# Optimization experiments

Measured on AMD Instinct MI355X. Metric: run time of the kernel, lower is better.

Reference implementation:

```python
import jax, jax.numpy as jnp
import numpy as np

B, L, D = 32, 512, 384
T_MAX = 4096
PAD_VALUE = 0.0
EXPAND_SCALE = 1.0


def setup_inputs() -> dict:
    key = jax.random.key(0)
    k1, k2, k3 = jax.random.split(key, 3)
    sequence = jax.random.normal(k1, (B, L, D), dtype=jnp.float32)
    duration = jax.random.randint(k2, (B, L), 0, 8, dtype=jnp.int64)
    padding_mask = jax.random.randint(k3, (B, L), 0, 2) == 1
    return {"sequence": sequence, "duration": duration,
            "padding_mask": padding_mask, "max_length": T_MAX}


def reference(sequence, duration, padding_mask, max_length):
    # expanded_duration = round(expand_scale * duration)
    exp_dur = jnp.round(EXPAND_SCALE * duration.astype(jnp.float32)).astype(jnp.int32)
    # mask padded tokens in the input sequence with pad_value
    seq = jnp.where(padding_mask[..., None], PAD_VALUE, sequence)  # (B, L, D)
    # cumulative durations: token t occupies output slots [cum[t-1], cum[t])
    cum = jnp.cumsum(exp_dur, axis=1)  # (B, L)
    pos = jnp.arange(max_length, dtype=cum.dtype)  # (T,)
    # idx[b, j] = first token index whose cumulative end exceeds j
    idx = jax.vmap(lambda c: jnp.searchsorted(c, pos, side="right"))(cum)  # (B, T)
    valid = pos[None, :] < cum[:, -1:]  # (B, T): within total expanded length
    idx = jnp.clip(idx, 0, seq.shape[1] - 1)
    out = jnp.take_along_axis(seq, idx[..., None], axis=1)  # (B, T, D)
    out = jnp.where(valid[..., None], out, PAD_VALUE)
    return out, exp_dur
```

## Files before the change

### kernel.cpp

```cpp
#include <hip/hip_runtime.h>

constexpr int B = 32;
constexpr int L = 512;
constexpr int D = 384;
constexpr int T = 4096;
constexpr int VPR = D / 4;
constexpr int OUT0 = B * T * D;
constexpr int RPB = 16;
constexpr int BLOCKS_PER_BATCH = T / RPB;
constexpr int NBLK = B * BLOCKS_PER_BATCH;
constexpr int BS = 256;
constexpr int PASSES = RPB * VPR / BS;

__global__ __launch_bounds__(L) void scan_k(const int* __restrict__ dur,
                                            int* __restrict__ cum,
                                            float* __restrict__ exp_dur_out) {
    const int b = blockIdx.x;
    const int t = threadIdx.x;
    __shared__ int s[L];
    int d = dur[b * L + t];
    exp_dur_out[b * L + t] = (float)d;
    s[t] = d;
    __syncthreads();
    #pragma unroll
    for (int off = 1; off < L; off <<= 1) {
        int v = (t >= off) ? s[t - off] : 0;
        __syncthreads();
        s[t] += v;
        __syncthreads();
    }
    cum[b * L + t] = s[t];
}

__global__ __launch_bounds__(BS) void fused_k(const float4* __restrict__ seq,
                                              const int* __restrict__ cum,
                                              const int* __restrict__ mask,
                                              float4* __restrict__ out) {
    __shared__ int s_cum[L];
    __shared__ int s_src[RPB];

    const int blk   = blockIdx.x;
    const int b     = blk >> 8;
    const int chunk = blk & 255;
    const int row0  = chunk * RPB;
    const int tid   = threadIdx.x;

    #pragma unroll
    for (int i = 0; i < L / BS; ++i)
        s_cum[i * BS + tid] = cum[b * L + i * BS + tid];
    __syncthreads();

    if (tid < RPB) {
        const int j = row0 + tid;
        const int total = s_cum[L - 1];
        int res = -1;
        if (j < total) {
            int lo = 0, hi = L;
            while (lo < hi) {
                int mid = (lo + hi) >> 1;
                if (s_cum[mid] <= j) lo = mid + 1; else hi = mid;
            }
            res = mask[b * L + lo] ? -1 : (b * L + lo);
        }
        s_src[tid] = res;
    }
    __syncthreads();

    float4* obase = out + (size_t)(b * T + row0) * VPR;
    #pragma unroll
    for (int p = 0; p < PASSES; ++p) {
        const int idx = p * BS + tid;
        const int r   = idx / VPR;
        const int col = idx - r * VPR;
        const int s   = s_src[r];
        float4 v = make_float4(0.f, 0.f, 0.f, 0.f);
        if (s >= 0) v = seq[(size_t)s * VPR + col];
        obase[idx] = v;
    }
}

extern "C" void kernel_launch(void* const* d_in, const int* in_sizes, int n_in,
                              void* d_out, int out_size, void* d_ws, size_t ws_size,
                              hipStream_t stream) {
    const float* seq  = (const float*)d_in[0];
    const int*   dur  = (const int*)d_in[1];
    const int*   mask = (const int*)d_in[2];

    float* out      = (float*)d_out;
    float* expd_out = out + OUT0;

    int* cum = (int*)d_ws;

    scan_k<<<B, L, 0, stream>>>(dur, cum, expd_out);
    fused_k<<<NBLK, BS, 0, stream>>>((const float4*)seq, cum, mask,
                                     (float4*)out);
}
```

Before: 217.5 us.

## Fuse duration scan into gather kernel with wave-shuffle scan and nontemporal stores

Removes the separate scan kernel. Each gather block now recomputes its batch's cumulative durations using a wave-level shuffle scan plus cross-wave offsets in shared memory, and caches the mask in shared memory. It also doubles rows per block, fully unrolls the binary search, and writes output with nontemporal stores. This saves one launch and the workspace round trip, at the cost of redundant per-block scans over duration and mask.

```diff
diff --git a/kernel.cpp b/kernel.cpp
--- a/kernel.cpp
+++ b/kernel.cpp
@@ -4,50 +4,57 @@
 constexpr int L = 512;
 constexpr int D = 384;
 constexpr int T = 4096;
-constexpr int VPR = D / 4;
+constexpr int VPR  = D / 4;
 constexpr int OUT0 = B * T * D;
-constexpr int RPB = 16;
-constexpr int BLOCKS_PER_BATCH = T / RPB;
-constexpr int NBLK = B * BLOCKS_PER_BATCH;
-constexpr int BS = 256;
+constexpr int BS   = 256;
+constexpr int RPB  = 32;
+constexpr int BPB  = T / RPB;
+constexpr int NBLK = B * BPB;
 constexpr int PASSES = RPB * VPR / BS;
+constexpr int NWAVE  = BS / 64;
 
-__global__ __launch_bounds__(L) void scan_k(const int* __restrict__ dur,
-                                            int* __restrict__ cum,
-                                            float* __restrict__ exp_dur_out) {
-    const int b = blockIdx.x;
-    const int t = threadIdx.x;
-    __shared__ int s[L];
-    int d = dur[b * L + t];
-    exp_dur_out[b * L + t] = (float)d;
-    s[t] = d;
-    __syncthreads();
-    #pragma unroll
-    for (int off = 1; off < L; off <<= 1) {
-        int v = (t >= off) ? s[t - off] : 0;
-        __syncthreads();
-        s[t] += v;
-        __syncthreads();
-    }
-    cum[b * L + t] = s[t];
-}
+typedef float v4f __attribute__((ext_vector_type(4)));
 
-__global__ __launch_bounds__(BS) void fused_k(const float4* __restrict__ seq,
-                                              const int* __restrict__ cum,
+__global__ __launch_bounds__(BS) void fused_k(const v4f* __restrict__ seq,
+                                              const int* __restrict__ dur,
                                               const int* __restrict__ mask,
-                                              float4* __restrict__ out) {
+                                              v4f*       __restrict__ out,
+                                              float*     __restrict__ expd) {
     __shared__ int s_cum[L];
+    __shared__ int s_mask[L];
+    __shared__ int s_wsum[NWAVE];
     __shared__ int s_src[RPB];
 
     const int blk   = blockIdx.x;
-    const int b     = blk >> 8;
-    const int chunk = blk & 255;
+    const int b     = blk >> 7;
+    const int chunk = blk & (BPB - 1);
     const int row0  = chunk * RPB;
     const int tid   = threadIdx.x;
+    const int lane  = tid & 63;
+    const int wave  = tid >> 6;
 
+    const int2 d2 = ((const int2*)(dur  + b * L))[tid];
+    const int2 m2 = ((const int2*)(mask + b * L))[tid];
+    const int e0 = d2.x, e1 = d2.y;
+
+    int v = e0 + e1;
     #pragma unroll
-    for (int i = 0; i < L / BS; ++i)
-        s_cum[i * BS + tid] = cum[b * L + i * BS + tid];
+    for (int off = 1; off < 64; off <<= 1) {
+        int u = __shfl_up(v, off, 64);
+        if (lane >= off) v += u;
+    }
+    if (lane == 63) s_wsum[wave] = v;
+    s_mask[2 * tid]     = m2.x;
+    s_mask[2 * tid + 1] = m2.y;
+    __syncthreads();
+
+    int woff = 0;
+    #pragma unroll
+    for (int w = 0; w < NWAVE; ++w)
+        if (w < wave) woff += s_wsum[w];
+    const int excl = v + woff - (e0 + e1);
+    s_cum[2 * tid]     = excl + e0;
+    s_cum[2 * tid + 1] = excl + e0 + e1;
     __syncthreads();
 
     if (tid < RPB) {
@@ -56,26 +63,32 @@
         int res = -1;
         if (j < total) {
             int lo = 0, hi = L;
-            while (lo < hi) {
+            #pragma unroll
+            for (int it = 0; it < 10; ++it) {
                 int mid = (lo + hi) >> 1;
                 if (s_cum[mid] <= j) lo = mid + 1; else hi = mid;
             }
-            res = mask[b * L + lo] ? -1 : (b * L + lo);
+            res = s_mask[lo] ? -1 : (b * L + lo);
         }
         s_src[tid] = res;
     }
     __syncthreads();
 
-    float4* obase = out + (size_t)(b * T + row0) * VPR;
+    v4f* obase = out + (size_t)(b * T + row0) * VPR;
     #pragma unroll
     for (int p = 0; p < PASSES; ++p) {
         const int idx = p * BS + tid;
         const int r   = idx / VPR;
         const int col = idx - r * VPR;
         const int s   = s_src[r];
-        float4 v = make_float4(0.f, 0.f, 0.f, 0.f);
-        if (s >= 0) v = seq[(size_t)s * VPR + col];
-        obase[idx] = v;
+        v4f vv = (v4f)(0.f);
+        if (s >= 0) vv = seq[s * VPR + col];
+        __builtin_nontemporal_store(vv, &obase[idx]);
+    }
+
+    if (chunk == 0) {
+        expd[b * L + 2 * tid]     = (float)e0;
+        expd[b * L + 2 * tid + 1] = (float)e1;
     }
 }
 
@@ -89,9 +102,6 @@
     float* out      = (float*)d_out;
     float* expd_out = out + OUT0;
 
-    int* cum = (int*)d_ws;
-
-    scan_k<<<B, L, 0, stream>>>(dur, cum, expd_out);
-    fused_k<<<NBLK, BS, 0, stream>>>((const float4*)seq, cum, mask,
-                                     (float4*)out);
+    fused_k<<<NBLK, BS, 0, stream>>>((const v4f*)seq, dur, mask,
+                                     (v4f*)out, expd_out);
 }
```

Measured after the change: 229.9 us. 5.7% more time.
